# Kernel optimization log

Hardware: AMD Instinct MI355X
Metric: run time of the kernel (lower is better)

## Reference

```python
import jax, jax.numpy as jnp
import numpy as np

N, E, G = 2048, 4096, 128      # nodes, edges, graphs
H, IN, ED = 128, 11, 4         # hidden, input node feat, edge feat
BN_EPS = 1e-5


def setup_inputs() -> dict:
    key = jax.random.key(0)
    ks = iter(jax.random.split(key, 40))
    r = lambda shape, s=0.1: jax.random.normal(next(ks), shape, jnp.float32) * s
    inp = dict(
        x=r((N, IN), 1.0),
        edge_attr=jax.random.uniform(next(ks), (E, ED), jnp.float32),
        edge_index=jax.random.randint(next(ks), (2, E), 0, N).astype(jnp.int32),
        batch=jnp.sort(jax.random.randint(next(ks), (N,), 0, G)).astype(jnp.int32),
        # layer 0 (in=11 -> out=128)
        w1_0=r((ED, H)), b1_0=jnp.zeros(H), w2_0=r((H, IN * H), 0.02), b2_0=jnp.zeros(IN * H),
        root_0=r((IN, H)), bias_0=jnp.zeros(H),
        bn_g0=jnp.ones(H), bn_b0=jnp.zeros(H), bn_m0=r((H,), 0.1),
        bn_v0=jax.random.uniform(next(ks), (H,), jnp.float32, 0.5, 1.5),
        # layers 1..4 stacked (in=out=128)
        w1_s=r((4, ED, H)), b1_s=jnp.zeros((4, H)), w2_s=r((4, H, H * H), 0.02), b2_s=jnp.zeros((4, H * H)),
        root_s=r((4, H, H)), bias_s=jnp.zeros((4, H)),
        bn_gs=jnp.ones((4, H)), bn_bs=jnp.zeros((4, H)), bn_ms=r((4, H), 0.1),
        bn_vs=jax.random.uniform(next(ks), (4, H), jnp.float32, 0.5, 1.5),
        # readout MLP
        lin1_w=r((H, H // 2)), lin1_b=jnp.zeros(H // 2),
        lin2_w=r((H // 2, 1)), lin2_b=jnp.zeros(1),
    )
    return inp


def _nnconv(x, src, dst, edge_attr, w1, b1, w2, b2, root, bias):
    in_c = x.shape[-1]
    h = jax.nn.relu(edge_attr @ w1 + b1)                 # [E, H]
    w_e = (h @ w2 + b2).reshape(-1, in_c, H)             # [E, in, H] per-edge weight
    msg = jnp.einsum('ei,eio->eo', x[src], w_e)          # gather + per-edge matvec
    s = jax.ops.segment_sum(msg, dst, num_segments=N)
    cnt = jax.ops.segment_sum(jnp.ones(dst.shape, x.dtype), dst, num_segments=N)
    aggr = s / jnp.maximum(cnt, 1.0)[:, None]            # scatter-mean
    return aggr + x @ root + bias


def _bn_eval(x, g, b, m, v):
    return (x - m) * jax.lax.rsqrt(v + BN_EPS) * g + b


def reference(x, edge_attr, w1_0, b1_0, w2_0, b2_0, root_0, bias_0,
              bn_g0, bn_b0, bn_m0, bn_v0,
              w1_s, b1_s, w2_s, b2_s, root_s, bias_s,
              bn_gs, bn_bs, bn_ms, bn_vs,
              lin1_w, lin1_b, lin2_w, lin2_b,
              edge_index, batch):
    src, dst = edge_index[0], edge_index[1]
    # layer 0
    h = jax.nn.relu(_bn_eval(
        _nnconv(x, src, dst, edge_attr, w1_0, b1_0, w2_0, b2_0, root_0, bias_0),
        bn_g0, bn_b0, bn_m0, bn_v0))
    # layers 1..4 with residual (dims match)
    for l in range(4):
        h_new = jax.nn.relu(_bn_eval(
            _nnconv(h, src, dst, edge_attr, w1_s[l], b1_s[l], w2_s[l], b2_s[l], root_s[l], bias_s[l]),
            bn_gs[l], bn_bs[l], bn_ms[l], bn_vs[l]))
        h = h + h_new
    # global mean pool over graphs
    gs = jax.ops.segment_sum(h, batch, num_segments=G)
    gc = jax.ops.segment_sum(jnp.ones((N,), h.dtype), batch, num_segments=G)
    g = gs / jnp.maximum(gc, 1.0)[:, None]
    # readout (dropout is identity in eval mode)
    g = jax.nn.relu(g @ lin1_w + lin1_b)
    return g @ lin2_w + lin2_b
```

## Files before the change

### kernel.cpp

```cpp
#include <hip/hip_runtime.h>
#include <cstdint>
#include <cstddef>

#define NN 2048
#define NE 4096
#define NG 128
#define HD 128
#define SKM 16
#define SK0 5
#define NCH 64
#define CHE 64

typedef unsigned short u16;
typedef __attribute__((ext_vector_type(8))) _Float16 f16x8;
typedef __attribute__((ext_vector_type(4))) float f32x4;

#define GLOAD_LDS16(gptr, lptr)                                                          \
  __builtin_amdgcn_global_load_lds((const __attribute__((address_space(1))) unsigned int*)(gptr), \
                                   (__attribute__((address_space(3))) unsigned int*)(lptr), 16, 0, 0)

__global__ void k_count(const int* __restrict__ dst, int* __restrict__ hist) {
  int e = blockIdx.x * 256 + threadIdx.x;
  if (e < NE) atomicAdd(&hist[(e >> 6) * NN + dst[e]], 1);
}

__global__ __launch_bounds__(1024) void k_scan2(const int* __restrict__ hist,
                                                int* __restrict__ rowptr,
                                                int* __restrict__ chunkoff,
                                                const int* __restrict__ batch,
                                                int* __restrict__ gstart) {
  __shared__ int s[NN];
  int t = threadIdx.x;
  int c0 = 0, c1 = 0;
  for (int c = 0; c < NCH; ++c) { c0 += hist[c * NN + t]; c1 += hist[c * NN + t + 1024]; }
  s[t] = c0; s[t + 1024] = c1;
  __syncthreads();
  for (int d = 1; d < NN; d <<= 1) {
    int a0 = s[t], a1 = s[t + 1024];
    int v0 = (t >= d) ? s[t - d] : 0;
    int v1 = (t + 1024 >= d) ? s[t + 1024 - d] : 0;
    __syncthreads();
    s[t] = a0 + v0; s[t + 1024] = a1 + v1;
    __syncthreads();
  }
  rowptr[t + 1] = s[t]; rowptr[t + 1025] = s[t + 1024];
  if (t == 0) rowptr[0] = 0;
  int run0 = s[t] - c0, run1 = s[t + 1024] - c1;
  for (int c = 0; c < NCH; ++c) {
    chunkoff[c * NN + t] = run0;        run0 += hist[c * NN + t];
    chunkoff[c * NN + t + 1024] = run1; run1 += hist[c * NN + t + 1024];
  }
  if (t <= NG) {
    int lo = 0, hi = NN;
    while (lo < hi) { int mid = (lo + hi) >> 1; if (batch[mid] < t) lo = mid + 1; else hi = mid; }
    gstart[t] = lo;
  }
}

__global__ __launch_bounds__(64) void k_fill2(const int* __restrict__ dst,
                                              const int* __restrict__ chunkoff,
                                              int* __restrict__ elist) {
  __shared__ int sd[CHE];
  int c = blockIdx.x, t = threadIdx.x;
  int e = c * CHE + t;
  int dv = dst[e];
  sd[t] = dv;
  __syncthreads();
  int lrank = 0;
  for (int j = 0; j < t; ++j) lrank += (sd[j] == dv) ? 1 : 0;
  elist[chunkoff[c * NN + dv] + lrank] = e;
}

__global__ void k_hallpad(const float* __restrict__ ea,
                          const float* __restrict__ w1_0, const float* __restrict__ b1_0,
                          const float* __restrict__ w1_s, const float* __restrict__ b1_s,
                          const float* __restrict__ x,
                          _Float16* __restrict__ hb, _Float16* __restrict__ x16) {
  int bid = blockIdx.x;
  if (bid < 10240) {
    int idx = bid * 256 + threadIdx.x;
    int c = idx & (HD - 1);
    int e = (idx >> 7) & (NE - 1);
    int l = idx >> 19;
    const float* w1 = (l == 0) ? w1_0 : (w1_s + (size_t)(l - 1) * 4 * HD);
    const float* b1 = (l == 0) ? b1_0 : (b1_s + (size_t)(l - 1) * HD);
    float4 a = *(const float4*)(ea + (size_t)e * 4);
    float v = b1[c] + a.x * w1[c] + a.y * w1[HD + c] + a.z * w1[2 * HD + c] + a.w * w1[3 * HD + c];
    hb[idx] = (_Float16)fmaxf(v, 0.f);
  } else {
    int idx = (bid - 10240) * 256 + threadIdx.x;
    int n = idx >> 4, i = idx & 15;
    x16[idx] = (_Float16)(i < 11 ? x[(size_t)n * 11 + i] : 0.f);
  }
}

__global__ __launch_bounds__(256) void k_w2t(const float* __restrict__ w2s,
                                             const float* __restrict__ b2s,
                                             _Float16* __restrict__ w2T) {
  int l = blockIdx.z;
  const float* w2 = w2s + (size_t)l * 16384 * 128;
  const float* b2 = b2s + (size_t)l * 128 * 128;
  _Float16* out = w2T + (size_t)l * 128 * 16512;
  __shared__ float s[64][65];
  int k0 = blockIdx.x * 64, o0 = blockIdx.y * 64;
  int t = threadIdx.x;
  int r = t >> 4, c = (t & 15) * 4;
#pragma unroll
  for (int it = 0; it < 4; ++it) {
    int kk = k0 + r + it * 16;
    const float* srcp = (kk < 16384) ? (w2 + (size_t)kk * 128 + o0 + c)
                                     : (b2 + (size_t)(kk - 16384) * 128 + o0 + c);
    *(float4*)&s[r + it * 16][c] = *(const float4*)srcp;
  }
  __syncthreads();
#pragma unroll
  for (int it = 0; it < 4; ++it) {
    int o = o0 + r + it * 16;
    _Float16 pk[4];
#pragma unroll
    for (int j = 0; j < 4; ++j) pk[j] = (_Float16)s[c + j][r + it * 16];
    *(unsigned long long*)(out + (size_t)o * 16512 + k0 + c) = *(const unsigned long long*)pk;
  }
}

__global__ void k_w2t0(const float* __restrict__ w2_0, const float* __restrict__ b2_0,
                       _Float16* __restrict__ w2T0) {
  int o = blockIdx.x, t = threadIdx.x;
  for (int kap = t; kap < 2080; kap += 256) {
    int k = kap >> 4, i = kap & 15;
    float v = 0.f;
    if (i < 11) {
      if (k < 128) v = w2_0[(size_t)k * 1408 + i * 128 + o];
      else if (k == 128) v = b2_0[i * 128 + o];
    }
    w2T0[(size_t)o * 2080 + kap] = (_Float16)v;
  }
}

template <bool L0>
__global__ __launch_bounds__(256, 2) void k_mma2(
    const _Float16* __restrict__ xh,
    const _Float16* __restrict__ hb,
    const _Float16* __restrict__ w2T,
    const int* __restrict__ src,
    _Float16* __restrict__ msgp) {
  constexpr int KT = L0 ? 2080 : 16512;
  constexpr int NWIN = L0 ? 1 : 4;
  __shared__ _Float16 Bs[2][4096];
  __shared__ _Float16 hTl[26][128];

  const int tid = threadIdx.x;
  const int e0 = blockIdx.x * 128;
  const int w = tid >> 6, l = tid & 63, l16 = l & 15, g = l >> 4;

  int k0, nk;
  if constexpr (L0) {
    k0 = blockIdx.y * 13; nk = 13;
  } else {
    int sk = blockIdx.y;
    if (sk == 0) { k0 = 0; nk = 9; } else { k0 = 9 + (sk - 1) * 8; nk = 8; }
  }
  const int kb = L0 ? k0 * 2 : k0;

  int nd[8];
#pragma unroll
  for (int mt = 0; mt < 8; ++mt) nd[mt] = src[e0 + mt * 16 + l16];

  {
    const int nrow = L0 ? 26 : nk;
    for (int idx = tid; idx < nrow * 128; idx += 256) {
      int kk = idx >> 7, m = idx & 127;
      int k = kb + kk;
      _Float16 v;
      if (k < 128) v = hb[(size_t)(e0 + m) * 128 + k];
      else v = (k == 128) ? (_Float16)1.0f : (_Float16)0.0f;
      hTl[kk][m] = v;
    }
  }

  auto stageB = [&](int buf, int kap0) {
#pragma unroll
    for (int j2 = 0; j2 < 2; ++j2) {
      int ntg = w * 2 + j2;
      const _Float16* gp = w2T + (size_t)(ntg * 16 + l16) * KT + kap0 + g * 8;
      GLOAD_LDS16(gp, &Bs[buf][(w * 128 + j2 * 64) * 8]);
    }
  };

  stageB(0, L0 ? k0 * 32 : k0 * 128);
  __syncthreads();

  f32x4 acc[8][2];
#pragma unroll
  for (int mt = 0; mt < 8; ++mt)
#pragma unroll
    for (int jj = 0; jj < 2; ++jj) acc[mt][jj] = (f32x4){0.f, 0.f, 0.f, 0.f};

  int buf = 0;
  for (int win = 0; win < NWIN; ++win) {
    f16x8 xw[8];
#pragma unroll
    for (int mt = 0; mt < 8; ++mt) {
      const _Float16* xp = L0 ? (xh + (size_t)nd[mt] * 16 + (g & 1) * 8)
                              : (xh + (size_t)nd[mt] * 128 + win * 32 + g * 8);
      xw[mt] = *(const f16x8*)xp;
    }
    for (int j = 0; j < nk; ++j) {
      const bool last = (j + 1 == nk) && (win + 1 == NWIN);
      if (j + 1 < nk) {
        stageB(buf ^ 1, L0 ? (k0 + j + 1) * 32 : (k0 + j + 1) * 128 + win * 32);
      } else if (win + 1 < NWIN) {
        stageB(buf ^ 1, k0 * 128 + (win + 1) * 32);
      }
      if (last) { asm volatile("s_waitcnt vmcnt(0)" ::: "memory"); }
      else      { asm volatile("s_waitcnt vmcnt(2)" ::: "memory"); }
      __builtin_amdgcn_sched_barrier(0);

      f16x8 bv0 = *(const f16x8*)&Bs[buf][(size_t)(w * 2 + 0) * 512 + l * 8];
      f16x8 bv1 = *(const f16x8*)&Bs[buf][(size_t)(w * 2 + 1) * 512 + l * 8];
#pragma unroll
      for (int mt = 0; mt < 8; ++mt) {
        _Float16 hh;
        if constexpr (L0) hh = hTl[2 * j + (g >> 1)][mt * 16 + l16];
        else              hh = hTl[j][mt * 16 + l16];
        f16x8 hv = {hh, hh, hh, hh, hh, hh, hh, hh};
        f16x8 av = xw[mt] * hv;
        acc[mt][0] = __builtin_amdgcn_mfma_f32_16x16x32_f16(av, bv0, acc[mt][0], 0, 0, 0);
        acc[mt][1] = __builtin_amdgcn_mfma_f32_16x16x32_f16(av, bv1, acc[mt][1], 0, 0, 0);
      }
      buf ^= 1;
    }
  }

  _Float16* mp = msgp + ((size_t)blockIdx.y * NE + e0) * 128;
#pragma unroll
  for (int mt = 0; mt < 8; ++mt)
#pragma unroll
    for (int jj = 0; jj < 2; ++jj)
#pragma unroll
      for (int r = 0; r < 4; ++r) {
        int row = mt * 16 + 4 * g + r;
        mp[(size_t)row * 128 + w * 32 + jj * 16 + l16] = (_Float16)acc[mt][jj][r];
      }
}

template <int INR, int NSK>
__global__ void k_au(const _Float16* __restrict__ msgp, const int* __restrict__ rowptr,
                     const int* __restrict__ elist, const float* __restrict__ xin,
                     const float* __restrict__ root, const float* __restrict__ bias,
                     const float* __restrict__ bg, const float* __restrict__ bb,
                     const float* __restrict__ bm, const float* __restrict__ bv,
                     const float* __restrict__ h_prev, float* __restrict__ h_out,
                     _Float16* __restrict__ h_out_h) {
  int n = blockIdx.x, t = threadIdx.x;
  __shared__ float xr[INR];
  if (t < INR) xr[t] = xin[(size_t)n * INR + t];
  int beg = rowptr[n], end = rowptr[n + 1];
  float v = 0.f;
  for (int j = beg; j < end; ++j) {
    int e = elist[j];
#pragma unroll
    for (int s = 0; s < NSK; ++s) v += (float)msgp[((size_t)s * NE + e) * HD + t];
  }
  v /= fmaxf((float)(end - beg), 1.f);
  __syncthreads();
  float acc = v + bias[t];
#pragma unroll 8
  for (int k = 0; k < INR; ++k) acc += xr[k] * root[(size_t)k * HD + t];
  float bn = (acc - bm[t]) * rsqrtf(bv[t] + 1e-5f) * bg[t] + bb[t];
  float r = fmaxf(bn, 0.f);
  float val = h_prev ? (h_prev[(size_t)n * HD + t] + r) : r;
  h_out[(size_t)n * HD + t] = val;
  h_out_h[(size_t)n * HD + t] = (_Float16)val;
}

__global__ void k_poolread(const float* __restrict__ h, const int* __restrict__ gstart,
                           const float* __restrict__ w1, const float* __restrict__ b1,
                           const float* __restrict__ w2, const float* __restrict__ b2,
                           float* __restrict__ out) {
  int g = blockIdx.x, t = threadIdx.x;
  __shared__ float row[HD];
  int beg = gstart[g], end = gstart[g + 1];
  float v = 0.f;
  for (int n = beg; n < end; ++n) v += h[(size_t)n * HD + t];
  row[t] = v / fmaxf((float)(end - beg), 1.f);
  __syncthreads();
  if (t < 64) {
    float acc = b1[t];
#pragma unroll 8
    for (int k = 0; k < HD; ++k) acc += row[k] * w1[(size_t)k * 64 + t];
    float vv = fmaxf(acc, 0.f) * w2[t];
#pragma unroll
    for (int off = 32; off > 0; off >>= 1) vv += __shfl_down(vv, off);
    if (t == 0) out[g] = vv + b2[0];
  }
}

extern "C" void kernel_launch(void* const* d_in, const int* in_sizes, int n_in,
                              void* d_out, int out_size, void* d_ws, size_t ws_size,
                              hipStream_t stream) {
  const float* x      = (const float*)d_in[0];
  const float* ea     = (const float*)d_in[1];
  const int*   eidx   = (const int*)d_in[2];
  const int*   batch  = (const int*)d_in[3];
  const float* w1_0   = (const float*)d_in[4];
  const float* b1_0   = (const float*)d_in[5];
  const float* w2_0   = (const float*)d_in[6];
  const float* b2_0   = (const float*)d_in[7];
  const float* root_0 = (const float*)d_in[8];
  const float* bias_0 = (const float*)d_in[9];
  const float* bn_g0  = (const float*)d_in[10];
  const float* bn_b0  = (const float*)d_in[11];
  const float* bn_m0  = (const float*)d_in[12];
  const float* bn_v0  = (const float*)d_in[13];
  const float* w1_s   = (const float*)d_in[14];
  const float* b1_s   = (const float*)d_in[15];
  const float* w2_s   = (const float*)d_in[16];
  const float* b2_s   = (const float*)d_in[17];
  const float* root_s = (const float*)d_in[18];
  const float* bias_s = (const float*)d_in[19];
  const float* bn_gs  = (const float*)d_in[20];
  const float* bn_bs  = (const float*)d_in[21];
  const float* bn_ms  = (const float*)d_in[22];
  const float* bn_vs  = (const float*)d_in[23];
  const float* lin1_w = (const float*)d_in[24];
  const float* lin1_b = (const float*)d_in[25];
  const float* lin2_w = (const float*)d_in[26];
  const float* lin2_b = (const float*)d_in[27];
  float* out = (float*)d_out;

  char* wsb = (char*)d_ws;
  size_t off = 0;
  auto alloc = [&](size_t bytes) { void* p = wsb + off; off = (off + bytes + 255) & ~(size_t)255; return p; };
  int*      rowptr   = (int*)alloc((NN + 4) * 4);
  int*      elist    = (int*)alloc(NE * 4);
  int*      gstart   = (int*)alloc((NG + 4) * 4);
  int*      hist     = (int*)alloc((size_t)NCH * NN * 4);
  int*      chunkoff = (int*)alloc((size_t)NCH * NN * 4);
  _Float16* hbf      = (_Float16*)alloc((size_t)5 * NE * HD * 2);
  _Float16* x16      = (_Float16*)alloc((size_t)NN * 16 * 2);
  _Float16* w2T0     = (_Float16*)alloc((size_t)128 * 2080 * 2);
  _Float16* w2T      = (_Float16*)alloc((size_t)4 * 128 * 16512 * 2);
  float*    hnA      = (float*)alloc((size_t)NN * HD * 4);
  float*    hnB      = (float*)alloc((size_t)NN * HD * 4);
  _Float16* hnAh     = (_Float16*)alloc((size_t)NN * HD * 2);
  _Float16* hnBh     = (_Float16*)alloc((size_t)NN * HD * 2);
  _Float16* msgp     = (_Float16*)alloc((size_t)SKM * NE * HD * 2);

  const int* src = eidx;
  const int* dstp = eidx + NE;

  hipMemsetAsync(hist, 0, (size_t)NCH * NN * 4, stream);
  k_count<<<dim3(16), 256, 0, stream>>>(dstp, hist);
  k_scan2<<<1, 1024, 0, stream>>>(hist, rowptr, chunkoff, batch, gstart);
  k_fill2<<<dim3(NCH), 64, 0, stream>>>(dstp, chunkoff, elist);
  k_hallpad<<<dim3(10368), 256, 0, stream>>>(ea, w1_0, b1_0, w1_s, b1_s, x, hbf, x16);
  k_w2t0<<<dim3(128), 256, 0, stream>>>(w2_0, b2_0, w2T0);
  k_w2t<<<dim3(16512 / 64, 2, 4), 256, 0, stream>>>(w2_s, b2_s, w2T);

  k_mma2<true><<<dim3(NE / 128, SK0), 256, 0, stream>>>(x16, hbf, w2T0, src, msgp);
  k_au<11, SK0><<<NN, HD, 0, stream>>>(msgp, rowptr, elist, x, root_0, bias_0,
                                       bn_g0, bn_b0, bn_m0, bn_v0, nullptr, hnA, hnAh);

  float* cur = hnA;  _Float16* curh = hnAh;
  float* nxt = hnB;  _Float16* nxth = hnBh;
  for (int l = 1; l <= 4; ++l) {
    const _Float16* w2Tl = w2T + (size_t)(l - 1) * 128 * 16512;
    k_mma2<false><<<dim3(NE / 128, SKM), 256, 0, stream>>>(
        curh, hbf + (size_t)l * NE * HD, w2Tl, src, msgp);
    k_au<128, SKM><<<NN, HD, 0, stream>>>(msgp, rowptr, elist, cur,
                                          root_s + (size_t)(l - 1) * HD * HD,
                                          bias_s + (size_t)(l - 1) * HD,
                                          bn_gs + (size_t)(l - 1) * HD, bn_bs + (size_t)(l - 1) * HD,
                                          bn_ms + (size_t)(l - 1) * HD, bn_vs + (size_t)(l - 1) * HD,
                                          cur, nxt, nxth);
    float* tf = cur; cur = nxt; nxt = tf;
    _Float16* th = curh; curh = nxth; nxth = th;
  }

  k_poolread<<<NG, HD, 0, stream>>>(cur, gstart, lin1_w, lin1_b, lin2_w, lin2_b, out);
}
```

Measured before the change: 255.7 us.

## Fuse preprocessing kernels and retile per-edge MMA to 256-edge, 512-thread blocks

Merges the count, h-precompute, x16 pad and both w2 transpose kernels into one launch, which cuts launch overhead and widens the transpose stores to 16 bytes. The hidden-layer MMA kernel becomes a 512-thread block covering 256 edges with 8 waves arranged 4 by 2. B tiles are streamed through a 4-deep LDS ring with prefetch distance 2, so each B tile is reused across twice as many edges and w2T traffic drops. The layer-0 kernel gains a per-step __syncthreads that guards its double buffer. In exchange, the grid shrinks to 256 blocks and the larger blocks need more registers and LDS.

```diff
diff --git a/kernel.cpp b/kernel.cpp
--- a/kernel.cpp
+++ b/kernel.cpp
@@ -11,7 +11,6 @@
 #define NCH 64
 #define CHE 64
 
-typedef unsigned short u16;
 typedef __attribute__((ext_vector_type(8))) _Float16 f16x8;
 typedef __attribute__((ext_vector_type(4))) float f32x4;
 
@@ -19,9 +18,76 @@
   __builtin_amdgcn_global_load_lds((const __attribute__((address_space(1))) unsigned int*)(gptr), \
                                    (__attribute__((address_space(3))) unsigned int*)(lptr), 16, 0, 0)
 
-__global__ void k_count(const int* __restrict__ dst, int* __restrict__ hist) {
-  int e = blockIdx.x * 256 + threadIdx.x;
-  if (e < NE) atomicAdd(&hist[(e >> 6) * NN + dst[e]], 1);
+__global__ __launch_bounds__(256) void k_prep(
+    const float* __restrict__ ea,
+    const float* __restrict__ w1_0, const float* __restrict__ b1_0,
+    const float* __restrict__ w1_s, const float* __restrict__ b1_s,
+    const float* __restrict__ x,
+    const float* __restrict__ w2_0, const float* __restrict__ b2_0,
+    const float* __restrict__ w2s, const float* __restrict__ b2s,
+    const int* __restrict__ dst, int* __restrict__ hist,
+    _Float16* __restrict__ hb, _Float16* __restrict__ x16,
+    _Float16* __restrict__ w2T0, _Float16* __restrict__ w2T) {
+  __shared__ float s[64][65];
+  const int bid = blockIdx.x, t = threadIdx.x;
+
+  if (bid < 10240) {
+    int idx = bid * 256 + t;
+    int c = idx & (HD - 1);
+    int e = (idx >> 7) & (NE - 1);
+    int l = idx >> 19;
+    const float* w1 = (l == 0) ? w1_0 : (w1_s + (size_t)(l - 1) * 4 * HD);
+    const float* b1 = (l == 0) ? b1_0 : (b1_s + (size_t)(l - 1) * HD);
+    float4 a = *(const float4*)(ea + (size_t)e * 4);
+    float v = b1[c] + a.x * w1[c] + a.y * w1[HD + c] + a.z * w1[2 * HD + c] + a.w * w1[3 * HD + c];
+    hb[idx] = (_Float16)fmaxf(v, 0.f);
+  } else if (bid < 10368) {
+    int idx = (bid - 10240) * 256 + t;
+    int n = idx >> 4, i = idx & 15;
+    x16[idx] = (_Float16)(i < 11 ? x[(size_t)n * 11 + i] : 0.f);
+  } else if (bid < 10496) {
+    int o = bid - 10368;
+    for (int kap = t; kap < 2080; kap += 256) {
+      int k = kap >> 4, i = kap & 15;
+      float v = 0.f;
+      if (i < 11) {
+        if (k < 128) v = w2_0[(size_t)k * 1408 + i * 128 + o];
+        else if (k == 128) v = b2_0[i * 128 + o];
+      }
+      w2T0[(size_t)o * 2080 + kap] = (_Float16)v;
+    }
+  } else if (bid < 12560) {
+    int idx2 = bid - 10496;
+    int l = idx2 / 516;
+    int rem = idx2 - l * 516;
+    int ob = rem / 258;
+    int kb = rem - ob * 258;
+    const float* w2 = w2s + (size_t)l * 16384 * 128;
+    const float* b2 = b2s + (size_t)l * 128 * 128;
+    _Float16* out = w2T + (size_t)l * 128 * 16512;
+    int k0 = kb * 64, o0 = ob * 64;
+    int r = t >> 4, c4 = (t & 15) * 4;
+#pragma unroll
+    for (int it = 0; it < 4; ++it) {
+      int kk = k0 + r + it * 16;
+      const float* srcp = (kk < 16384) ? (w2 + (size_t)kk * 128 + o0 + c4)
+                                       : (b2 + (size_t)(kk - 16384) * 128 + o0 + c4);
+      *(float4*)&s[r + it * 16][c4] = *(const float4*)srcp;
+    }
+    __syncthreads();
+    int rr = t >> 3, c8 = (t & 7) * 8;
+#pragma unroll
+    for (int it = 0; it < 2; ++it) {
+      int ol = rr + it * 32;
+      _Float16 pk[8];
+#pragma unroll
+      for (int j = 0; j < 8; ++j) pk[j] = (_Float16)s[c8 + j][ol];
+      *(f16x8*)(out + (size_t)(o0 + ol) * 16512 + k0 + c8) = *(const f16x8*)pk;
+    }
+  } else {
+    int e = (bid - 12560) * 256 + t;
+    if (e < NE) atomicAdd(&hist[(e >> 6) * NN + dst[e]], 1);
+  }
 }
 
 __global__ __launch_bounds__(1024) void k_scan2(const int* __restrict__ hist,
@@ -71,81 +137,13 @@
   elist[chunkoff[c * NN + dv] + lrank] = e;
 }
 
-__global__ void k_hallpad(const float* __restrict__ ea,
-                          const float* __restrict__ w1_0, const float* __restrict__ b1_0,
-                          const float* __restrict__ w1_s, const float* __restrict__ b1_s,
-                          const float* __restrict__ x,
-                          _Float16* __restrict__ hb, _Float16* __restrict__ x16) {
-  int bid = blockIdx.x;
-  if (bid < 10240) {
-    int idx = bid * 256 + threadIdx.x;
-    int c = idx & (HD - 1);
-    int e = (idx >> 7) & (NE - 1);
-    int l = idx >> 19;
-    const float* w1 = (l == 0) ? w1_0 : (w1_s + (size_t)(l - 1) * 4 * HD);
-    const float* b1 = (l == 0) ? b1_0 : (b1_s + (size_t)(l - 1) * HD);
-    float4 a = *(const float4*)(ea + (size_t)e * 4);
-    float v = b1[c] + a.x * w1[c] + a.y * w1[HD + c] + a.z * w1[2 * HD + c] + a.w * w1[3 * HD + c];
-    hb[idx] = (_Float16)fmaxf(v, 0.f);
-  } else {
-    int idx = (bid - 10240) * 256 + threadIdx.x;
-    int n = idx >> 4, i = idx & 15;
-    x16[idx] = (_Float16)(i < 11 ? x[(size_t)n * 11 + i] : 0.f);
-  }
-}
-
-__global__ __launch_bounds__(256) void k_w2t(const float* __restrict__ w2s,
-                                             const float* __restrict__ b2s,
-                                             _Float16* __restrict__ w2T) {
-  int l = blockIdx.z;
-  const float* w2 = w2s + (size_t)l * 16384 * 128;
-  const float* b2 = b2s + (size_t)l * 128 * 128;
-  _Float16* out = w2T + (size_t)l * 128 * 16512;
-  __shared__ float s[64][65];
-  int k0 = blockIdx.x * 64, o0 = blockIdx.y * 64;
-  int t = threadIdx.x;
-  int r = t >> 4, c = (t & 15) * 4;
-#pragma unroll
-  for (int it = 0; it < 4; ++it) {
-    int kk = k0 + r + it * 16;
-    const float* srcp = (kk < 16384) ? (w2 + (size_t)kk * 128 + o0 + c)
-                                     : (b2 + (size_t)(kk - 16384) * 128 + o0 + c);
-    *(float4*)&s[r + it * 16][c] = *(const float4*)srcp;
-  }
-  __syncthreads();
-#pragma unroll
-  for (int it = 0; it < 4; ++it) {
-    int o = o0 + r + it * 16;
-    _Float16 pk[4];
-#pragma unroll
-    for (int j = 0; j < 4; ++j) pk[j] = (_Float16)s[c + j][r + it * 16];
-    *(unsigned long long*)(out + (size_t)o * 16512 + k0 + c) = *(const unsigned long long*)pk;
-  }
-}
-
-__global__ void k_w2t0(const float* __restrict__ w2_0, const float* __restrict__ b2_0,
-                       _Float16* __restrict__ w2T0) {
-  int o = blockIdx.x, t = threadIdx.x;
-  for (int kap = t; kap < 2080; kap += 256) {
-    int k = kap >> 4, i = kap & 15;
-    float v = 0.f;
-    if (i < 11) {
-      if (k < 128) v = w2_0[(size_t)k * 1408 + i * 128 + o];
-      else if (k == 128) v = b2_0[i * 128 + o];
-    }
-    w2T0[(size_t)o * 2080 + kap] = (_Float16)v;
-  }
-}
-
-template <bool L0>
-__global__ __launch_bounds__(256, 2) void k_mma2(
+__global__ __launch_bounds__(256, 2) void k_mma0(
     const _Float16* __restrict__ xh,
     const _Float16* __restrict__ hb,
     const _Float16* __restrict__ w2T,
     const int* __restrict__ src,
     _Float16* __restrict__ msgp) {
-  constexpr int KT = L0 ? 2080 : 16512;
-  constexpr int NWIN = L0 ? 1 : 4;
+  constexpr int KT = 2080;
   __shared__ _Float16 Bs[2][4096];
   __shared__ _Float16 hTl[26][128];
 
@@ -153,32 +151,29 @@
   const int e0 = blockIdx.x * 128;
   const int w = tid >> 6, l = tid & 63, l16 = l & 15, g = l >> 4;
 
-  int k0, nk;
-  if constexpr (L0) {
-    k0 = blockIdx.y * 13; nk = 13;
-  } else {
-    int sk = blockIdx.y;
-    if (sk == 0) { k0 = 0; nk = 9; } else { k0 = 9 + (sk - 1) * 8; nk = 8; }
-  }
-  const int kb = L0 ? k0 * 2 : k0;
+  const int k0 = blockIdx.y * 13, nk = 13;
+  const int kb = k0 * 2;
 
   int nd[8];
 #pragma unroll
   for (int mt = 0; mt < 8; ++mt) nd[mt] = src[e0 + mt * 16 + l16];
 
-  {
-    const int nrow = L0 ? 26 : nk;
-    for (int idx = tid; idx < nrow * 128; idx += 256) {
-      int kk = idx >> 7, m = idx & 127;
-      int k = kb + kk;
-      _Float16 v;
-      if (k < 128) v = hb[(size_t)(e0 + m) * 128 + k];
-      else v = (k == 128) ? (_Float16)1.0f : (_Float16)0.0f;
-      hTl[kk][m] = v;
-    }
-  }
-
-  auto stageB = [&](int buf, int kap0) {
+  for (int idx = tid; idx < 26 * 128; idx += 256) {
+    int kk = idx >> 7, m = idx & 127;
+    int k = kb + kk;
+    _Float16 v;
+    if (k < 128) v = hb[(size_t)(e0 + m) * 128 + k];
+    else v = (k == 128) ? (_Float16)1.0f : (_Float16)0.0f;
+    hTl[kk][m] = v;
+  }
+
+  f16x8 xr[8];
+#pragma unroll
+  for (int mt = 0; mt < 8; ++mt)
+    xr[mt] = *(const f16x8*)(xh + (size_t)nd[mt] * 16 + (g & 1) * 8);
+
+  auto stageB = [&](int buf, int c) {
+    const int kap0 = c * 32;
 #pragma unroll
     for (int j2 = 0; j2 < 2; ++j2) {
       int ntg = w * 2 + j2;
@@ -187,7 +182,7 @@
     }
   };
 
-  stageB(0, L0 ? k0 * 32 : k0 * 128);
+  stageB(0, k0);
   __syncthreads();
 
   f32x4 acc[8][2];
@@ -197,39 +192,27 @@
     for (int jj = 0; jj < 2; ++jj) acc[mt][jj] = (f32x4){0.f, 0.f, 0.f, 0.f};
 
   int buf = 0;
-  for (int win = 0; win < NWIN; ++win) {
-    f16x8 xw[8];
+  for (int j = 0; j < nk; ++j) {
+    if (j + 1 < nk) {
+      stageB(buf ^ 1, k0 + j + 1);
+      asm volatile("s_waitcnt vmcnt(2)" ::: "memory");
+    } else {
+      asm volatile("s_waitcnt vmcnt(0)" ::: "memory");
+    }
+    __builtin_amdgcn_sched_barrier(0);
+
+    f16x8 bv0 = *(const f16x8*)&Bs[buf][(size_t)(w * 2 + 0) * 512 + l * 8];
+    f16x8 bv1 = *(const f16x8*)&Bs[buf][(size_t)(w * 2 + 1) * 512 + l * 8];
 #pragma unroll
     for (int mt = 0; mt < 8; ++mt) {
-      const _Float16* xp = L0 ? (xh + (size_t)nd[mt] * 16 + (g & 1) * 8)
-                              : (xh + (size_t)nd[mt] * 128 + win * 32 + g * 8);
-      xw[mt] = *(const f16x8*)xp;
-    }
-    for (int j = 0; j < nk; ++j) {
-      const bool last = (j + 1 == nk) && (win + 1 == NWIN);
-      if (j + 1 < nk) {
-        stageB(buf ^ 1, L0 ? (k0 + j + 1) * 32 : (k0 + j + 1) * 128 + win * 32);
-      } else if (win + 1 < NWIN) {
-        stageB(buf ^ 1, k0 * 128 + (win + 1) * 32);
-      }
-      if (last) { asm volatile("s_waitcnt vmcnt(0)" ::: "memory"); }
-      else      { asm volatile("s_waitcnt vmcnt(2)" ::: "memory"); }
-      __builtin_amdgcn_sched_barrier(0);
-
-      f16x8 bv0 = *(const f16x8*)&Bs[buf][(size_t)(w * 2 + 0) * 512 + l * 8];
-      f16x8 bv1 = *(const f16x8*)&Bs[buf][(size_t)(w * 2 + 1) * 512 + l * 8];
-#pragma unroll
-      for (int mt = 0; mt < 8; ++mt) {
-        _Float16 hh;
-        if constexpr (L0) hh = hTl[2 * j + (g >> 1)][mt * 16 + l16];
-        else              hh = hTl[j][mt * 16 + l16];
-        f16x8 hv = {hh, hh, hh, hh, hh, hh, hh, hh};
-        f16x8 av = xw[mt] * hv;
-        acc[mt][0] = __builtin_amdgcn_mfma_f32_16x16x32_f16(av, bv0, acc[mt][0], 0, 0, 0);
-        acc[mt][1] = __builtin_amdgcn_mfma_f32_16x16x32_f16(av, bv1, acc[mt][1], 0, 0, 0);
-      }
-      buf ^= 1;
-    }
+      _Float16 hh = hTl[2 * j + (g >> 1)][mt * 16 + l16];
+      f16x8 hv = {hh, hh, hh, hh, hh, hh, hh, hh};
+      f16x8 av = xr[mt] * hv;
+      acc[mt][0] = __builtin_amdgcn_mfma_f32_16x16x32_f16(av, bv0, acc[mt][0], 0, 0, 0);
+      acc[mt][1] = __builtin_amdgcn_mfma_f32_16x16x32_f16(av, bv1, acc[mt][1], 0, 0, 0);
+    }
+    buf ^= 1;
+    __syncthreads();
   }
 
   _Float16* mp = msgp + ((size_t)blockIdx.y * NE + e0) * 128;
@@ -241,6 +224,109 @@
       for (int r = 0; r < 4; ++r) {
         int row = mt * 16 + 4 * g + r;
         mp[(size_t)row * 128 + w * 32 + jj * 16 + l16] = (_Float16)acc[mt][jj][r];
+      }
+}
+
+__global__ __launch_bounds__(512, 2) void k_mma3(
+    const _Float16* __restrict__ xh,
+    const _Float16* __restrict__ hb,
+    const _Float16* __restrict__ w2T,
+    const int* __restrict__ src,
+    _Float16* __restrict__ msgp) {
+  constexpr int KT = 16512;
+  __shared__ __align__(16) _Float16 Bs[4][4096];
+  __shared__ _Float16 hTl[9][256];
+
+  const int tid = threadIdx.x;
+  const int w = tid >> 6, l = tid & 63, l16 = l & 15, g = l >> 4;
+  const int bid = blockIdx.x;
+  const int eb = bid >> 4, sk = bid & 15;
+  const int e0 = eb * 256;
+  const int mg = w & 3, ng = w >> 2;
+
+  int k0, nk;
+  if (sk == 0) { k0 = 0; nk = 9; } else { k0 = 9 + (sk - 1) * 8; nk = 8; }
+  const int nsteps = nk * 4;
+
+  auto stageB = [&](int s) {
+    const int jk = s >> 2, win = s & 3;
+    const int kap0 = (k0 + jk) * 128 + win * 32;
+    const _Float16* gp = w2T + (size_t)(w * 16 + l16) * KT + kap0 + g * 8;
+    GLOAD_LDS16(gp, &Bs[s & 3][w * 512]);
+  };
+
+  stageB(0);
+  stageB(1);
+
+  int nd[4];
+#pragma unroll
+  for (int mt = 0; mt < 4; ++mt) nd[mt] = src[e0 + mg * 64 + mt * 16 + l16];
+  f16x8 xw[4][4];
+#pragma unroll
+  for (int mt = 0; mt < 4; ++mt)
+#pragma unroll
+    for (int win = 0; win < 4; ++win)
+      xw[mt][win] = *(const f16x8*)(xh + (size_t)nd[mt] * 128 + win * 32 + g * 8);
+
+  for (int idx = tid; idx < nk * 256; idx += 512) {
+    int jk = idx >> 8, m = idx & 255;
+    int k = k0 + jk;
+    hTl[jk][m] = (k < 128) ? hb[(size_t)(e0 + m) * 128 + k]
+                           : (_Float16)(k == 128 ? 1.0f : 0.0f);
+  }
+  __syncthreads();
+
+  f32x4 acc[4][4];
+#pragma unroll
+  for (int mt = 0; mt < 4; ++mt)
+#pragma unroll
+    for (int j2 = 0; j2 < 4; ++j2) acc[mt][j2] = (f32x4){0.f, 0.f, 0.f, 0.f};
+
+  for (int jk = 0; jk < nk; ++jk) {
+    _Float16 hv[4];
+#pragma unroll
+    for (int mt = 0; mt < 4; ++mt) hv[mt] = hTl[jk][mg * 64 + mt * 16 + l16];
+#pragma unroll
+    for (int win = 0; win < 4; ++win) {
+      const int s = jk * 4 + win;
+      if (s + 2 < nsteps) {
+        stageB(s + 2);
+        asm volatile("s_waitcnt vmcnt(2)" ::: "memory");
+      } else if (s + 2 == nsteps) {
+        asm volatile("s_waitcnt vmcnt(1)" ::: "memory");
+      } else {
+        asm volatile("s_waitcnt vmcnt(0)" ::: "memory");
+      }
+      __builtin_amdgcn_s_barrier();
+
+      const _Float16* bp = &Bs[win][ng * 2048 + g * 128 + l16 * 8];
+      f16x8 bv0 = *(const f16x8*)(bp);
+      f16x8 bv1 = *(const f16x8*)(bp + 512);
+      f16x8 bv2 = *(const f16x8*)(bp + 1024);
+      f16x8 bv3 = *(const f16x8*)(bp + 1536);
+#pragma unroll
+      for (int mt = 0; mt < 4; ++mt) {
+        _Float16 hh = hv[mt];
+        f16x8 hs = {hh, hh, hh, hh, hh, hh, hh, hh};
+        f16x8 av = xw[mt][win] * hs;
+        acc[mt][0] = __builtin_amdgcn_mfma_f32_16x16x32_f16(av, bv0, acc[mt][0], 0, 0, 0);
+        acc[mt][1] = __builtin_amdgcn_mfma_f32_16x16x32_f16(av, bv1, acc[mt][1], 0, 0, 0);
+        acc[mt][2] = __builtin_amdgcn_mfma_f32_16x16x32_f16(av, bv2, acc[mt][2], 0, 0, 0);
+        acc[mt][3] = __builtin_amdgcn_mfma_f32_16x16x32_f16(av, bv3, acc[mt][3], 0, 0, 0);
+      }
+    }
+  }
+
+  _Float16* mp = msgp + ((size_t)sk * NE + e0) * 128;
+#pragma unroll
+  for (int mt = 0; mt < 4; ++mt)
+#pragma unroll
+    for (int j2 = 0; j2 < 4; ++j2)
+#pragma unroll
+      for (int r = 0; r < 4; ++r) {
+        int row = mg * 64 + mt * 16 + 4 * g + r;
+        int col = (ng * 4 + j2) * 16 + l16;
+        mp[(size_t)row * 128 + col] = (_Float16)acc[mt][j2][r];
       }
 }
 
@@ -351,14 +437,13 @@
   const int* dstp = eidx + NE;
 
   hipMemsetAsync(hist, 0, (size_t)NCH * NN * 4, stream);
-  k_count<<<dim3(16), 256, 0, stream>>>(dstp, hist);
+  k_prep<<<dim3(12576), 256, 0, stream>>>(ea, w1_0, b1_0, w1_s, b1_s, x,
+                                          w2_0, b2_0, w2_s, b2_s,
+                                          dstp, hist, hbf, x16, w2T0, w2T);
   k_scan2<<<1, 1024, 0, stream>>>(hist, rowptr, chunkoff, batch, gstart);
   k_fill2<<<dim3(NCH), 64, 0, stream>>>(dstp, chunkoff, elist);
-  k_hallpad<<<dim3(10368), 256, 0, stream>>>(ea, w1_0, b1_0, w1_s, b1_s, x, hbf, x16);
-  k_w2t0<<<dim3(128), 256, 0, stream>>>(w2_0, b2_0, w2T0);
-  k_w2t<<<dim3(16512 / 64, 2, 4), 256, 0, stream>>>(w2_s, b2_s, w2T);
-
-  k_mma2<true><<<dim3(NE / 128, SK0), 256, 0, stream>>>(x16, hbf, w2T0, src, msgp);
+
+  k_mma0<<<dim3(NE / 128, SK0), 256, 0, stream>>>(x16, hbf, w2T0, src, msgp);
   k_au<11, SK0><<<NN, HD, 0, stream>>>(msgp, rowptr, elist, x, root_0, bias_0,
                                        bn_g0, bn_b0, bn_m0, bn_v0, nullptr, hnA, hnAh);
 
@@ -366,8 +451,7 @@
   float* nxt = hnB;  _Float16* nxth = hnBh;
   for (int l = 1; l <= 4; ++l) {
     const _Float16* w2Tl = w2T + (size_t)(l - 1) * 128 * 16512;
-    k_mma2<false><<<dim3(NE / 128, SKM), 256, 0, stream>>>(
-        curh, hbf + (size_t)l * NE * HD, w2Tl, src, msgp);
+    k_mma3<<<dim3(256), 512, 0, stream>>>(curh, hbf + (size_t)l * NE * HD, w2Tl, src, msgp);
     k_au<128, SKM><<<NN, HD, 0, stream>>>(msgp, rowptr, elist, cur,
                                           root_s + (size_t)(l - 1) * HD * HD,
                                           bias_s + (size_t)(l - 1) * HD,
```

Result: faster. 237.3 us (-7.2%).
